# Kernel tuning notes

Measured on AMD Instinct MI355X. Metric: run time of the kernel, lower is better.

The kernel has to match this reference:

```python
import jax, jax.numpy as jnp
import numpy as np

B, N, D, H = 2, 2048, 1024, 16
DK = D // H
SCALE = DK ** -0.5


def setup_inputs() -> dict:
    key = jax.random.key(0)
    ks = jax.random.split(key, 11)
    s = D ** -0.5
    return {
        "q": jax.random.normal(ks[0], (B, N, D), jnp.float32),
        "k": jax.random.normal(ks[1], (B, N, D), jnp.float32),
        "v": jax.random.normal(ks[2], (B, N, D), jnp.float32),
        "Wq": jax.random.normal(ks[3], (D, D), jnp.float32) * s,
        "bq": jnp.zeros((D,), jnp.float32),
        "Wk": jax.random.normal(ks[4], (D, D), jnp.float32) * s,
        "bk": jnp.zeros((D,), jnp.float32),
        "Wv": jax.random.normal(ks[5], (D, D), jnp.float32) * s,
        "bv": jnp.zeros((D,), jnp.float32),
        "Wo": jax.random.normal(ks[6], (D, D), jnp.float32) * s,
        "bo": jnp.zeros((D,), jnp.float32),
    }


def _split_heads(x):
    # [b, n, h*d] -> [b, h, n, d]
    b, n, _ = x.shape
    return x.reshape(b, n, H, DK).transpose(0, 2, 1, 3)


def reference(q, k, v, Wq, bq, Wk, bk, Wv, bv, Wo, bo):
    qh = _split_heads(q @ Wq.T + bq)
    kh = _split_heads(k @ Wk.T + bk)
    vh = _split_heads(v @ Wv.T + bv)
    dots = jnp.einsum('bhid,bhjd->bhij', qh, kh) * SCALE
    attn = jax.nn.softmax(dots, axis=-1)
    out = jnp.einsum('bhij,bhjd->bhid', attn, vh)
    out = out.transpose(0, 2, 1, 3).reshape(q.shape[0], q.shape[1], D)
    return out @ Wo.T + bo
```

## Files before the change

kernel.cpp:

```cpp
#include <hip/hip_runtime.h>
#include <hip/hip_bf16.h>
#include <cstdint>
#include <cstddef>

#define BB 2
#define NN 2048
#define DD 1024
#define HH 16
#define DKK 64
#define SCALE 0.125f
#define LOG2E 1.4426950408889634f

typedef __bf16 bf16;
typedef __bf16 bf16x4 __attribute__((ext_vector_type(4)));
typedef __bf16 bf16x8 __attribute__((ext_vector_type(8)));
typedef float f32x4 __attribute__((ext_vector_type(4)));
typedef short s16x4 __attribute__((ext_vector_type(4)));

#define GLD(gp, lp)                                                            \
  __builtin_amdgcn_global_load_lds(                                            \
      (const __attribute__((address_space(1))) void*)(gp),                     \
      (__attribute__((address_space(3))) void*)(lp), 16, 0, 0)

struct CvtArgs { const float* s[4]; bf16* d[4]; };

__global__ void k_cvtN(CvtArgs a, int n) {
  const float* __restrict__ s = a.s[blockIdx.y];
  bf16* __restrict__ d = a.d[blockIdx.y];
  int i = (blockIdx.x * 256 + threadIdx.x) * 4;
  if (i >= n) return;
  float4 f = *(const float4*)(s + i);
  bf16x4 o;
  o.x = (bf16)f.x; o.y = (bf16)f.y; o.z = (bf16)f.z; o.w = (bf16)f.w;
  *(bf16x4*)(d + i) = o;
}

__device__ __forceinline__ void gemm_body(
    const bf16* __restrict__ A, const bf16* __restrict__ W,
    const float* __restrict__ bias, bf16* __restrict__ outB,
    float* __restrict__ outF, int mode, int m0, int n0) {
  const int K = 1024;
  __shared__ bf16 lA[128 * 32];
  __shared__ bf16 lB[128 * 32];
  const int t = threadIdx.x;
  const int lane = t & 63;
  const int quad = lane >> 4;
  const int l16 = lane & 15;
  const int w = t >> 6;
  const int wm = (w >> 1) * 64;
  const int wn = (w & 1) * 64;

  f32x4 acc[4][4] = {};

  int i0 = t, i1 = t + 256;
  int r0 = i0 >> 2, c0 = (i0 & 3) ^ (r0 & 3);
  int r1 = i1 >> 2, c1 = (i1 & 3) ^ (r1 & 3);
  const bf16* gA0 = A + (size_t)(m0 + r0) * K + c0 * 8;
  const bf16* gA1 = A + (size_t)(m0 + r1) * K + c1 * 8;
  const bf16* gB0 = W + (size_t)(n0 + r0) * K + c0 * 8;
  const bf16* gB1 = W + (size_t)(n0 + r1) * K + c1 * 8;

  const int swzA = (quad ^ (l16 & 3)) * 8;

  for (int kb = 0; kb < K; kb += 32) {
    __syncthreads();
    GLD(gA0 + kb, lA + i0 * 8);
    GLD(gA1 + kb, lA + i1 * 8);
    GLD(gB0 + kb, lB + i0 * 8);
    GLD(gB1 + kb, lB + i1 * 8);
    __syncthreads();

    bf16x8 af[4], bf[4];
#pragma unroll
    for (int i = 0; i < 4; i++) {
      af[i] = *(const bf16x8*)(lA + (wm + i * 16 + l16) * 32 + swzA);
      bf[i] = *(const bf16x8*)(lB + (wn + i * 16 + l16) * 32 + swzA);
    }
#pragma unroll
    for (int mi = 0; mi < 4; mi++)
#pragma unroll
      for (int ni = 0; ni < 4; ni++)
        acc[mi][ni] = __builtin_amdgcn_mfma_f32_16x16x32_bf16(
            af[mi], bf[ni], acc[mi][ni], 0, 0, 0);
  }

#pragma unroll
  for (int mi = 0; mi < 4; mi++) {
#pragma unroll
    for (int ni = 0; ni < 4; ni++) {
#pragma unroll
      for (int r = 0; r < 4; r++) {
        int gm = m0 + wm + mi * 16 + quad * 4 + r;
        int gn = n0 + wn + ni * 16 + l16;
        float v = acc[mi][ni][r] + bias[gn];
        if (mode == 3) {
          outF[(size_t)gm * 1024 + gn] = v;
        } else {
          int b = gm >> 11, row = gm & 2047;
          int h = gn >> 6, dk = gn & 63;
          if (mode == 2)
            outB[((size_t)(b * HH + h) * DKK + dk) * NN + row] = (bf16)v;
          else
            outB[((size_t)(b * HH + h) * NN + row) * DKK + dk] = (bf16)v;
        }
      }
    }
  }
}

__global__ __launch_bounds__(256, 2) void k_gemm(
    const bf16* __restrict__ A, const bf16* __restrict__ W,
    const float* __restrict__ bias, bf16* __restrict__ outB,
    float* __restrict__ outF, int mode) {
  gemm_body(A, W, bias, outB, outF, mode, blockIdx.y * 128, blockIdx.x * 128);
}

struct GemmArgs { const bf16* A[3]; const bf16* W[3]; const float* b[3]; bf16* o[3]; };

__global__ __launch_bounds__(256, 2) void k_gemm3(GemmArgs g) {
  int z = blockIdx.z;
  gemm_body(g.A[z], g.W[z], g.b[z], g.o[z], nullptr, z == 2 ? 2 : 0,
            blockIdx.y * 128, blockIdx.x * 128);
}

__global__ __launch_bounds__(256, 2) void k_attn(
    const bf16* __restrict__ Qp, const bf16* __restrict__ Kp,
    const bf16* __restrict__ Vt, bf16* __restrict__ Ao) {
  __shared__ bf16 lK[128 * 64];
  __shared__ bf16 lV[64 * 128];
  const int t = threadIdx.x;
  const int lane = t & 63;
  const int quad = lane >> 4;
  const int l16 = lane & 15;
  const int w = t >> 6;
  const int bh = blockIdx.y;
  const int qt = blockIdx.x;
  const bf16* Qb = Qp + (size_t)bh * NN * DKK;
  const bf16* Kb = Kp + (size_t)bh * NN * DKK;
  const bf16* Vb = Vt + (size_t)bh * DKK * NN;

  const int qr0 = qt * 128 + w * 32;
  bf16x8 qf[2][2];
#pragma unroll
  for (int j = 0; j < 2; j++)
#pragma unroll
    for (int kq = 0; kq < 2; kq++)
      qf[j][kq] = *(const bf16x8*)(Qb + (size_t)(qr0 + j * 16 + l16) * DKK +
                                   kq * 32 + quad * 8);

  float mj[2] = {-3.0e38f, -3.0e38f}, lj[2] = {0.f, 0.f};
  f32x4 oacc[2][4] = {};
  const float c = SCALE * LOG2E;

  const bf16* gK[4]; const bf16* gV[4];
#pragma unroll
  for (int i4 = 0; i4 < 4; i4++) {
    int i = i4 * 256 + t;
    int rK = i >> 3, cK = (i & 7) ^ (rK & 7);
    gK[i4] = Kb + (size_t)rK * DKK + cK * 8;
    int rV = i >> 4, cV = (i & 15) ^ (rV & 15);
    gV[i4] = Vb + (size_t)rV * NN + cV * 8;
  }
  const int swzK0 = ((quad) ^ (l16 & 7)) * 8;
  const int swzK1 = ((4 + quad) ^ (l16 & 7)) * 8;

  for (int kt = 0; kt < NN; kt += 128) {
    __syncthreads();
#pragma unroll
    for (int i4 = 0; i4 < 4; i4++) {
      GLD(gK[i4] + (size_t)kt * DKK, lK + (i4 * 256 + t) * 8);
      GLD(gV[i4] + kt, lV + (i4 * 256 + t) * 8);
    }
    __syncthreads();

    f32x4 s[2][8];
#pragma unroll
    for (int tt = 0; tt < 8; tt++) {
      const bf16* kbase = lK + (tt * 16 + l16) * 64;
      bf16x8 kf0 = *(const bf16x8*)(kbase + swzK0);
      bf16x8 kf1 = *(const bf16x8*)(kbase + swzK1);
#pragma unroll
      for (int j = 0; j < 2; j++) {
        f32x4 z = {0.f, 0.f, 0.f, 0.f};
        z = __builtin_amdgcn_mfma_f32_16x16x32_bf16(kf0, qf[j][0], z, 0, 0, 0);
        z = __builtin_amdgcn_mfma_f32_16x16x32_bf16(kf1, qf[j][1], z, 0, 0, 0);
        s[j][tt] = z;
      }
    }

    s16x4 pa[2][8];
#pragma unroll
    for (int j = 0; j < 2; j++) {
      float mx = -3.0e38f;
#pragma unroll
      for (int tt = 0; tt < 8; tt++)
#pragma unroll
        for (int r = 0; r < 4; r++) mx = fmaxf(mx, s[j][tt][r]);
      mx = fmaxf(mx, __shfl_xor(mx, 16));
      mx = fmaxf(mx, __shfl_xor(mx, 32));
      float mn = fmaxf(mj[j], mx);
      float al = __builtin_amdgcn_exp2f((mj[j] - mn) * c);
      mj[j] = mn;
      float rs = 0.f;
#pragma unroll
      for (int tt = 0; tt < 8; tt++) {
        bf16x4 pb;
#pragma unroll
        for (int r = 0; r < 4; r++) {
          float p = __builtin_amdgcn_exp2f((s[j][tt][r] - mn) * c);
          rs += p;
          pb[r] = (bf16)p;
        }
        pa[j][tt] = __builtin_bit_cast(s16x4, pb);
      }
      rs += __shfl_xor(rs, 16);
      rs += __shfl_xor(rs, 32);
      lj[j] = lj[j] * al + rs;
      float alr[4];
#pragma unroll
      for (int r = 0; r < 4; r++) alr[r] = __shfl(al, quad * 4 + r);
#pragma unroll
      for (int ni = 0; ni < 4; ni++)
#pragma unroll
        for (int r = 0; r < 4; r++) oacc[j][ni][r] *= alr[r];
    }

#pragma unroll
    for (int tt = 0; tt < 8; tt++) {
#pragma unroll
      for (int ni = 0; ni < 4; ni++) {
        int rv = ni * 16 + l16;
        int cc = 2 * tt + (quad >> 1);
        const bf16* vaddr =
            lV + rv * 128 + ((cc ^ l16) * 8) + (quad & 1) * 4;
        s16x4 vb = __builtin_bit_cast(s16x4, *(const bf16x4*)vaddr);
#pragma unroll
        for (int j = 0; j < 2; j++)
          oacc[j][ni] = __builtin_amdgcn_mfma_f32_16x16x16bf16_1k(
              pa[j][tt], vb, oacc[j][ni], 0, 0, 0);
      }
    }
  }

  const int b = bh >> 4, h = bh & 15;
#pragma unroll
  for (int j = 0; j < 2; j++) {
    float inv[4];
#pragma unroll
    for (int r = 0; r < 4; r++) inv[r] = 1.0f / __shfl(lj[j], quad * 4 + r);
#pragma unroll
    for (int ni = 0; ni < 4; ni++)
#pragma unroll
      for (int r = 0; r < 4; r++) {
        int row = qr0 + j * 16 + quad * 4 + r;
        Ao[(size_t)(b * NN + row) * DD + h * DKK + ni * 16 + l16] =
            (bf16)(oacc[j][ni][r] * inv[r]);
      }
  }
}

extern "C" void kernel_launch(void* const* d_in, const int* in_sizes, int n_in,
                              void* d_out, int out_size, void* d_ws,
                              size_t ws_size, hipStream_t stream) {
  const float* qin = (const float*)d_in[0];
  const float* kin = (const float*)d_in[1];
  const float* vin = (const float*)d_in[2];
  const float* Wq = (const float*)d_in[3];
  const float* bq = (const float*)d_in[4];
  const float* Wk = (const float*)d_in[5];
  const float* bk = (const float*)d_in[6];
  const float* Wv = (const float*)d_in[7];
  const float* bv = (const float*)d_in[8];
  const float* Wo = (const float*)d_in[9];
  const float* bo = (const float*)d_in[10];
  float* out = (float*)d_out;

  const int MN = BB * NN * DD;
  const int WNel = DD * DD;
  bf16* ws = (bf16*)d_ws;

  if (ws_size >= (size_t)(3 * MN + 4 * WNel + 3 * MN) * sizeof(bf16)) {
    bf16* xq = ws;
    bf16* xk = xq + MN;
    bf16* xv = xk + MN;
    bf16* wqb = xv + MN;
    bf16* wkb = wqb + WNel;
    bf16* wvb = wkb + WNel;
    bf16* wob = wvb + WNel;
    bf16* Qp = wob + WNel;
    bf16* Kp = Qp + MN;
    bf16* Vt = Kp + MN;
    bf16* Ao = xq;

    CvtArgs ci{{qin, kin, vin, nullptr}, {xq, xk, xv, nullptr}};
    k_cvtN<<<dim3(MN / 1024, 3), 256, 0, stream>>>(ci, MN);
    CvtArgs cw{{Wq, Wk, Wv, Wo}, {wqb, wkb, wvb, wob}};
    k_cvtN<<<dim3(WNel / 1024, 4), 256, 0, stream>>>(cw, WNel);

    GemmArgs g{{xq, xk, xv}, {wqb, wkb, wvb}, {bq, bk, bv}, {Qp, Kp, Vt}};
    k_gemm3<<<dim3(8, 32, 3), 256, 0, stream>>>(g);

    k_attn<<<dim3(16, 32), 256, 0, stream>>>(Qp, Kp, Vt, Ao);
    k_gemm<<<dim3(8, 32), 256, 0, stream>>>(Ao, wob, bo, nullptr, out, 3);
  } else {
    bf16* xb = ws;
    bf16* wqb = xb + MN;
    bf16* wkb = wqb + WNel;
    bf16* wvb = wkb + WNel;
    bf16* wob = wvb + WNel;
    bf16* Qp = wob + WNel;
    bf16* Kp = Qp + MN;
    bf16* Vt = Kp + MN;

    CvtArgs cw{{Wq, Wk, Wv, Wo}, {wqb, wkb, wvb, wob}};
    k_cvtN<<<dim3(WNel / 1024, 4), 256, 0, stream>>>(cw, WNel);

    CvtArgs c0{{qin, nullptr, nullptr, nullptr}, {xb, nullptr, nullptr, nullptr}};
    k_cvtN<<<dim3(MN / 1024, 1), 256, 0, stream>>>(c0, MN);
    k_gemm<<<dim3(8, 32), 256, 0, stream>>>(xb, wqb, bq, Qp, nullptr, 0);
    CvtArgs c1{{kin, nullptr, nullptr, nullptr}, {xb, nullptr, nullptr, nullptr}};
    k_cvtN<<<dim3(MN / 1024, 1), 256, 0, stream>>>(c1, MN);
    k_gemm<<<dim3(8, 32), 256, 0, stream>>>(xb, wkb, bk, Kp, nullptr, 0);
    CvtArgs c2{{vin, nullptr, nullptr, nullptr}, {xb, nullptr, nullptr, nullptr}};
    k_cvtN<<<dim3(MN / 1024, 1), 256, 0, stream>>>(c2, MN);
    k_gemm<<<dim3(8, 32), 256, 0, stream>>>(xb, wvb, bv, Vt, nullptr, 2);

    k_attn<<<dim3(16, 32), 256, 0, stream>>>(Qp, Kp, Vt, xb);
    k_gemm<<<dim3(8, 32), 256, 0, stream>>>(xb, wob, bo, nullptr, out, 3);
  }
}
```

Measured before the change: 252.9 us.

## Fuse fp32-to-bf16 conversion into GEMMs, double-buffer GEMM and attention

The separate conversion kernels are removed. GEMMs now load fp32 activations and weights, convert them to bf16 in registers and store them into double-buffered LDS with a software prefetch. The softmax scale times log2e is folded into the Q projection output. Attention moves to 512-thread blocks with 16 query rows per wave, double-buffered K/V tiles, a transposed MFMA so each lane writes vectorized output, and a swapped grid order. The output projection uses 128x64 tiles. This removes the conversion passes and exposes more overlap, at the cost of more VGPR and LDS pressure and fp32 weight reads repeated across tiles.

```diff
diff --git a/kernel.cpp b/kernel.cpp
--- a/kernel.cpp
+++ b/kernel.cpp
@@ -22,77 +22,115 @@
       (const __attribute__((address_space(1))) void*)(gp),                     \
       (__attribute__((address_space(3))) void*)(lp), 16, 0, 0)
 
-struct CvtArgs { const float* s[4]; bf16* d[4]; };
-
-__global__ void k_cvtN(CvtArgs a, int n) {
-  const float* __restrict__ s = a.s[blockIdx.y];
-  bf16* __restrict__ d = a.d[blockIdx.y];
-  int i = (blockIdx.x * 256 + threadIdx.x) * 4;
-  if (i >= n) return;
-  float4 f = *(const float4*)(s + i);
-  bf16x4 o;
-  o.x = (bf16)f.x; o.y = (bf16)f.y; o.z = (bf16)f.z; o.w = (bf16)f.w;
-  *(bf16x4*)(d + i) = o;
-}
-
+__device__ __forceinline__ bf16x8 cvt8(float4 a, float4 b) {
+  bf16x8 o;
+  o[0] = (bf16)a.x; o[1] = (bf16)a.y; o[2] = (bf16)a.z; o[3] = (bf16)a.w;
+  o[4] = (bf16)b.x; o[5] = (bf16)b.y; o[6] = (bf16)b.z; o[7] = (bf16)b.w;
+  return o;
+}
+
+template <bool AF32, int BN>
 __device__ __forceinline__ void gemm_body(
-    const bf16* __restrict__ A, const bf16* __restrict__ W,
+    const void* Aptr, const float* __restrict__ Wf,
     const float* __restrict__ bias, bf16* __restrict__ outB,
-    float* __restrict__ outF, int mode, int m0, int n0) {
+    float* __restrict__ outF, int mode, float oscale, int m0, int n0) {
   const int K = 1024;
-  __shared__ bf16 lA[128 * 32];
-  __shared__ bf16 lB[128 * 32];
+  constexpr int NI = BN / 32;
+  __shared__ bf16 lA[2][128 * 32];
+  __shared__ bf16 lB[2][BN * 32];
   const int t = threadIdx.x;
-  const int lane = t & 63;
-  const int quad = lane >> 4;
-  const int l16 = lane & 15;
-  const int w = t >> 6;
-  const int wm = (w >> 1) * 64;
-  const int wn = (w & 1) * 64;
-
-  f32x4 acc[4][4] = {};
-
-  int i0 = t, i1 = t + 256;
-  int r0 = i0 >> 2, c0 = (i0 & 3) ^ (r0 & 3);
-  int r1 = i1 >> 2, c1 = (i1 & 3) ^ (r1 & 3);
-  const bf16* gA0 = A + (size_t)(m0 + r0) * K + c0 * 8;
-  const bf16* gA1 = A + (size_t)(m0 + r1) * K + c1 * 8;
-  const bf16* gB0 = W + (size_t)(n0 + r0) * K + c0 * 8;
-  const bf16* gB1 = W + (size_t)(n0 + r1) * K + c1 * 8;
-
-  const int swzA = (quad ^ (l16 & 3)) * 8;
-
+  const int lane = t & 63, quad = lane >> 4, l16 = lane & 15, w = t >> 6;
+  const int wm = (w >> 1) * 64, wn = (w & 1) * (BN / 2);
+
+  f32x4 acc[4][NI] = {};
+
+  const float* Af = (const float*)Aptr;
+  const bf16* Ab = (const bf16*)Aptr;
+  const int rA = t >> 1, cA = (t & 1) * 16;
+  const int iA0 = t, iA1 = t + 256;
+  const int rG0 = iA0 >> 2, cG0 = (iA0 & 3) ^ (rG0 & 3);
+  const int rG1 = iA1 >> 2, cG1 = (iA1 & 3) ^ (rG1 & 3);
+  const int rW = (BN == 128) ? (t >> 1) : (t >> 2);
+  const int cW = (BN == 128) ? ((t & 1) * 16) : ((t & 3) * 8);
+
+  float4 ar[4];
+  float4 wr[BN == 128 ? 4 : 2];
+
+  auto issueA = [&](int kb, int pp) {
+    if constexpr (AF32) {
+#pragma unroll
+      for (int i = 0; i < 4; i++)
+        ar[i] = *(const float4*)(Af + (size_t)(m0 + rA) * K + kb + cA + i * 4);
+    } else {
+      GLD(Ab + (size_t)(m0 + rG0) * K + kb + cG0 * 8, &lA[pp][iA0 * 8]);
+      GLD(Ab + (size_t)(m0 + rG1) * K + kb + cG1 * 8, &lA[pp][iA1 * 8]);
+    }
+  };
+  auto writeA = [&](int pp) {
+    if constexpr (AF32) {
+      bf16x8 w0 = cvt8(ar[0], ar[1]), w1 = cvt8(ar[2], ar[3]);
+      const int ch0 = cA >> 3;
+      *(bf16x8*)&lA[pp][rA * 32 + ((ch0 ^ (rA & 3)) * 8)] = w0;
+      *(bf16x8*)&lA[pp][rA * 32 + (((ch0 + 1) ^ (rA & 3)) * 8)] = w1;
+    }
+  };
+  auto loadW = [&](int kb) {
+#pragma unroll
+    for (int i = 0; i < (BN == 128 ? 4 : 2); i++)
+      wr[i] = *(const float4*)(Wf + (size_t)(n0 + rW) * K + kb + cW + i * 4);
+  };
+  auto writeW = [&](int pp) {
+    if constexpr (BN == 128) {
+      bf16x8 w0 = cvt8(wr[0], wr[1]), w1 = cvt8(wr[2], wr[3]);
+      const int ch0 = cW >> 3;
+      *(bf16x8*)&lB[pp][rW * 32 + ((ch0 ^ (rW & 3)) * 8)] = w0;
+      *(bf16x8*)&lB[pp][rW * 32 + (((ch0 + 1) ^ (rW & 3)) * 8)] = w1;
+    } else {
+      bf16x8 w0 = cvt8(wr[0], wr[1]);
+      *(bf16x8*)&lB[pp][rW * 32 + ((((cW >> 3)) ^ (rW & 3)) * 8)] = w0;
+    }
+  };
+
+  issueA(0, 0);
+  loadW(0);
+  writeA(0);
+  writeW(0);
+  __syncthreads();
+
+  const int swz = (quad ^ (l16 & 3)) * 8;
+  int p = 0;
   for (int kb = 0; kb < K; kb += 32) {
+    const bool more = kb + 32 < K;
+    if (more) { issueA(kb + 32, p ^ 1); loadW(kb + 32); }
+
+    bf16x8 af[4], bfr[NI];
+#pragma unroll
+    for (int i = 0; i < 4; i++)
+      af[i] = *(const bf16x8*)&lA[p][(wm + i * 16 + l16) * 32 + swz];
+#pragma unroll
+    for (int i = 0; i < NI; i++)
+      bfr[i] = *(const bf16x8*)&lB[p][(wn + i * 16 + l16) * 32 + swz];
+#pragma unroll
+    for (int mi = 0; mi < 4; mi++)
+#pragma unroll
+      for (int ni = 0; ni < NI; ni++)
+        acc[mi][ni] = __builtin_amdgcn_mfma_f32_16x16x32_bf16(
+            af[mi], bfr[ni], acc[mi][ni], 0, 0, 0);
+
+    if (more) { writeA(p ^ 1); writeW(p ^ 1); }
     __syncthreads();
-    GLD(gA0 + kb, lA + i0 * 8);
-    GLD(gA1 + kb, lA + i1 * 8);
-    GLD(gB0 + kb, lB + i0 * 8);
-    GLD(gB1 + kb, lB + i1 * 8);
-    __syncthreads();
-
-    bf16x8 af[4], bf[4];
-#pragma unroll
-    for (int i = 0; i < 4; i++) {
-      af[i] = *(const bf16x8*)(lA + (wm + i * 16 + l16) * 32 + swzA);
-      bf[i] = *(const bf16x8*)(lB + (wn + i * 16 + l16) * 32 + swzA);
-    }
-#pragma unroll
-    for (int mi = 0; mi < 4; mi++)
-#pragma unroll
-      for (int ni = 0; ni < 4; ni++)
-        acc[mi][ni] = __builtin_amdgcn_mfma_f32_16x16x32_bf16(
-            af[mi], bf[ni], acc[mi][ni], 0, 0, 0);
+    p ^= 1;
   }
 
 #pragma unroll
   for (int mi = 0; mi < 4; mi++) {
 #pragma unroll
-    for (int ni = 0; ni < 4; ni++) {
+    for (int ni = 0; ni < NI; ni++) {
 #pragma unroll
       for (int r = 0; r < 4; r++) {
         int gm = m0 + wm + mi * 16 + quad * 4 + r;
         int gn = n0 + wn + ni * 16 + l16;
-        float v = acc[mi][ni][r] + bias[gn];
+        float v = (acc[mi][ni][r] + bias[gn]) * oscale;
         if (mode == 3) {
           outF[(size_t)gm * 1024 + gn] = v;
         } else {
@@ -108,122 +146,120 @@
   }
 }
 
-__global__ __launch_bounds__(256, 2) void k_gemm(
-    const bf16* __restrict__ A, const bf16* __restrict__ W,
-    const float* __restrict__ bias, bf16* __restrict__ outB,
-    float* __restrict__ outF, int mode) {
-  gemm_body(A, W, bias, outB, outF, mode, blockIdx.y * 128, blockIdx.x * 128);
-}
-
-struct GemmArgs { const bf16* A[3]; const bf16* W[3]; const float* b[3]; bf16* o[3]; };
-
-__global__ __launch_bounds__(256, 2) void k_gemm3(GemmArgs g) {
-  int z = blockIdx.z;
-  gemm_body(g.A[z], g.W[z], g.b[z], g.o[z], nullptr, z == 2 ? 2 : 0,
-            blockIdx.y * 128, blockIdx.x * 128);
-}
-
-__global__ __launch_bounds__(256, 2) void k_attn(
+struct QkvArgs {
+  const float* A[3]; const float* W[3]; const float* b[3]; bf16* o[3];
+  float sc[3];
+};
+
+__global__ __launch_bounds__(256, 3) void k_qkv(QkvArgs g) {
+  const int z = blockIdx.z;
+  gemm_body<true, 128>(g.A[z], g.W[z], g.b[z], g.o[z], nullptr,
+                       z == 2 ? 2 : 0, g.sc[z], blockIdx.x * 128,
+                       blockIdx.y * 128);
+}
+
+__global__ __launch_bounds__(256, 3) void k_oproj(
+    const bf16* __restrict__ A, const float* __restrict__ W,
+    const float* __restrict__ bias, float* __restrict__ out) {
+  gemm_body<false, 64>(A, W, bias, nullptr, out, 3, 1.0f, blockIdx.x * 128,
+                       blockIdx.y * 64);
+}
+
+__global__ __launch_bounds__(512, 4) void k_attn(
     const bf16* __restrict__ Qp, const bf16* __restrict__ Kp,
     const bf16* __restrict__ Vt, bf16* __restrict__ Ao) {
-  __shared__ bf16 lK[128 * 64];
-  __shared__ bf16 lV[64 * 128];
+  __shared__ bf16 lK[2][128 * 64];
+  __shared__ bf16 lV[2][64 * 128];
   const int t = threadIdx.x;
-  const int lane = t & 63;
-  const int quad = lane >> 4;
-  const int l16 = lane & 15;
-  const int w = t >> 6;
-  const int bh = blockIdx.y;
-  const int qt = blockIdx.x;
+  const int lane = t & 63, quad = lane >> 4, l16 = lane & 15, w = t >> 6;
+  const int bh = blockIdx.x;
+  const int qt = blockIdx.y;
   const bf16* Qb = Qp + (size_t)bh * NN * DKK;
   const bf16* Kb = Kp + (size_t)bh * NN * DKK;
   const bf16* Vb = Vt + (size_t)bh * DKK * NN;
 
-  const int qr0 = qt * 128 + w * 32;
-  bf16x8 qf[2][2];
-#pragma unroll
-  for (int j = 0; j < 2; j++)
-#pragma unroll
-    for (int kq = 0; kq < 2; kq++)
-      qf[j][kq] = *(const bf16x8*)(Qb + (size_t)(qr0 + j * 16 + l16) * DKK +
-                                   kq * 32 + quad * 8);
-
-  float mj[2] = {-3.0e38f, -3.0e38f}, lj[2] = {0.f, 0.f};
-  f32x4 oacc[2][4] = {};
-  const float c = SCALE * LOG2E;
-
-  const bf16* gK[4]; const bf16* gV[4];
-#pragma unroll
-  for (int i4 = 0; i4 < 4; i4++) {
-    int i = i4 * 256 + t;
+  const int qr0 = qt * 128 + w * 16;
+  bf16x8 qf[2];
+#pragma unroll
+  for (int kq = 0; kq < 2; kq++)
+    qf[kq] = *(const bf16x8*)(Qb + (size_t)(qr0 + l16) * DKK + kq * 32 +
+                              quad * 8);
+
+  float mj = -3.0e38f, lj = 0.f;
+  f32x4 oaccT[4] = {};
+
+  const bf16* gK[2]; const bf16* gV[2];
+#pragma unroll
+  for (int i2 = 0; i2 < 2; i2++) {
+    int i = i2 * 512 + t;
     int rK = i >> 3, cK = (i & 7) ^ (rK & 7);
-    gK[i4] = Kb + (size_t)rK * DKK + cK * 8;
+    gK[i2] = Kb + (size_t)rK * DKK + cK * 8;
     int rV = i >> 4, cV = (i & 15) ^ (rV & 15);
-    gV[i4] = Vb + (size_t)rV * NN + cV * 8;
-  }
-  const int swzK0 = ((quad) ^ (l16 & 7)) * 8;
+    gV[i2] = Vb + (size_t)rV * NN + cV * 8;
+  }
+  const int swzK0 = (quad ^ (l16 & 7)) * 8;
   const int swzK1 = ((4 + quad) ^ (l16 & 7)) * 8;
 
+#pragma unroll
+  for (int i2 = 0; i2 < 2; i2++) {
+    GLD(gK[i2], &lK[0][(i2 * 512 + t) * 8]);
+    GLD(gV[i2], &lV[0][(i2 * 512 + t) * 8]);
+  }
+
+  int p = 0;
   for (int kt = 0; kt < NN; kt += 128) {
     __syncthreads();
-#pragma unroll
-    for (int i4 = 0; i4 < 4; i4++) {
-      GLD(gK[i4] + (size_t)kt * DKK, lK + (i4 * 256 + t) * 8);
-      GLD(gV[i4] + kt, lV + (i4 * 256 + t) * 8);
-    }
-    __syncthreads();
-
-    f32x4 s[2][8];
+    if (kt + 128 < NN) {
+#pragma unroll
+      for (int i2 = 0; i2 < 2; i2++) {
+        GLD(gK[i2] + (size_t)(kt + 128) * DKK, &lK[p ^ 1][(i2 * 512 + t) * 8]);
+        GLD(gV[i2] + (kt + 128), &lV[p ^ 1][(i2 * 512 + t) * 8]);
+      }
+    }
+
+    f32x4 s[8];
 #pragma unroll
     for (int tt = 0; tt < 8; tt++) {
-      const bf16* kbase = lK + (tt * 16 + l16) * 64;
+      const bf16* kbase = &lK[p][(tt * 16 + l16) * 64];
       bf16x8 kf0 = *(const bf16x8*)(kbase + swzK0);
       bf16x8 kf1 = *(const bf16x8*)(kbase + swzK1);
-#pragma unroll
-      for (int j = 0; j < 2; j++) {
-        f32x4 z = {0.f, 0.f, 0.f, 0.f};
-        z = __builtin_amdgcn_mfma_f32_16x16x32_bf16(kf0, qf[j][0], z, 0, 0, 0);
-        z = __builtin_amdgcn_mfma_f32_16x16x32_bf16(kf1, qf[j][1], z, 0, 0, 0);
-        s[j][tt] = z;
+      f32x4 z = {0.f, 0.f, 0.f, 0.f};
+      z = __builtin_amdgcn_mfma_f32_16x16x32_bf16(kf0, qf[0], z, 0, 0, 0);
+      z = __builtin_amdgcn_mfma_f32_16x16x32_bf16(kf1, qf[1], z, 0, 0, 0);
+      s[tt] = z;
+    }
+
+    float mx = -3.0e38f;
+#pragma unroll
+    for (int tt = 0; tt < 8; tt++)
+#pragma unroll
+      for (int r = 0; r < 4; r++) mx = fmaxf(mx, s[tt][r]);
+    mx = fmaxf(mx, __shfl_xor(mx, 16));
+    mx = fmaxf(mx, __shfl_xor(mx, 32));
+    float mn = fmaxf(mj, mx);
+    float al = __builtin_amdgcn_exp2f(mj - mn);
+    mj = mn;
+
+    float rs = 0.f;
+    s16x4 pa[8];
+#pragma unroll
+    for (int tt = 0; tt < 8; tt++) {
+      bf16x4 pb;
+#pragma unroll
+      for (int r = 0; r < 4; r++) {
+        float pe = __builtin_amdgcn_exp2f(s[tt][r] - mn);
+        rs += pe;
+        pb[r] = (bf16)pe;
       }
-    }
-
-    s16x4 pa[2][8];
-#pragma unroll
-    for (int j = 0; j < 2; j++) {
-      float mx = -3.0e38f;
-#pragma unroll
-      for (int tt = 0; tt < 8; tt++)
-#pragma unroll
-        for (int r = 0; r < 4; r++) mx = fmaxf(mx, s[j][tt][r]);
-      mx = fmaxf(mx, __shfl_xor(mx, 16));
-      mx = fmaxf(mx, __shfl_xor(mx, 32));
-      float mn = fmaxf(mj[j], mx);
-      float al = __builtin_amdgcn_exp2f((mj[j] - mn) * c);
-      mj[j] = mn;
-      float rs = 0.f;
-#pragma unroll
-      for (int tt = 0; tt < 8; tt++) {
-        bf16x4 pb;
-#pragma unroll
-        for (int r = 0; r < 4; r++) {
-          float p = __builtin_amdgcn_exp2f((s[j][tt][r] - mn) * c);
-          rs += p;
-          pb[r] = (bf16)p;
-        }
-        pa[j][tt] = __builtin_bit_cast(s16x4, pb);
-      }
-      rs += __shfl_xor(rs, 16);
-      rs += __shfl_xor(rs, 32);
-      lj[j] = lj[j] * al + rs;
-      float alr[4];
-#pragma unroll
-      for (int r = 0; r < 4; r++) alr[r] = __shfl(al, quad * 4 + r);
-#pragma unroll
-      for (int ni = 0; ni < 4; ni++)
-#pragma unroll
-        for (int r = 0; r < 4; r++) oacc[j][ni][r] *= alr[r];
-    }
+      pa[tt] = __builtin_bit_cast(s16x4, pb);
+    }
+    rs += __shfl_xor(rs, 16);
+    rs += __shfl_xor(rs, 32);
+    lj = lj * al + rs;
+#pragma unroll
+    for (int ni = 0; ni < 4; ni++)
+#pragma unroll
+      for (int r = 0; r < 4; r++) oaccT[ni][r] *= al;
 
 #pragma unroll
     for (int tt = 0; tt < 8; tt++) {
@@ -232,30 +268,24 @@
         int rv = ni * 16 + l16;
         int cc = 2 * tt + (quad >> 1);
         const bf16* vaddr =
-            lV + rv * 128 + ((cc ^ l16) * 8) + (quad & 1) * 4;
+            &lV[p][rv * 128 + ((cc ^ l16) * 8) + (quad & 1) * 4];
         s16x4 vb = __builtin_bit_cast(s16x4, *(const bf16x4*)vaddr);
-#pragma unroll
-        for (int j = 0; j < 2; j++)
-          oacc[j][ni] = __builtin_amdgcn_mfma_f32_16x16x16bf16_1k(
-              pa[j][tt], vb, oacc[j][ni], 0, 0, 0);
+        oaccT[ni] = __builtin_amdgcn_mfma_f32_16x16x16bf16_1k(vb, pa[tt],
+                                                              oaccT[ni], 0, 0, 0);
       }
     }
-  }
-
+    p ^= 1;
+  }
+
+  const float inv = 1.0f / lj;
   const int b = bh >> 4, h = bh & 15;
-#pragma unroll
-  for (int j = 0; j < 2; j++) {
-    float inv[4];
-#pragma unroll
-    for (int r = 0; r < 4; r++) inv[r] = 1.0f / __shfl(lj[j], quad * 4 + r);
-#pragma unroll
-    for (int ni = 0; ni < 4; ni++)
-#pragma unroll
-      for (int r = 0; r < 4; r++) {
-        int row = qr0 + j * 16 + quad * 4 + r;
-        Ao[(size_t)(b * NN + row) * DD + h * DKK + ni * 16 + l16] =
-            (bf16)(oacc[j][ni][r] * inv[r]);
-      }
+  bf16* dst = Ao + ((size_t)(b * NN) + qr0 + l16) * DD + h * DKK + quad * 4;
+#pragma unroll
+  for (int ni = 0; ni < 4; ni++) {
+    bf16x4 ov;
+#pragma unroll
+    for (int r = 0; r < 4; r++) ov[r] = (bf16)(oaccT[ni][r] * inv);
+    *(bf16x4*)(dst + ni * 16) = ov;
   }
 }
 
@@ -276,56 +306,16 @@
   float* out = (float*)d_out;
 
   const int MN = BB * NN * DD;
-  const int WNel = DD * DD;
   bf16* ws = (bf16*)d_ws;
-
-  if (ws_size >= (size_t)(3 * MN + 4 * WNel + 3 * MN) * sizeof(bf16)) {
-    bf16* xq = ws;
-    bf16* xk = xq + MN;
-    bf16* xv = xk + MN;
-    bf16* wqb = xv + MN;
-    bf16* wkb = wqb + WNel;
-    bf16* wvb = wkb + WNel;
-    bf16* wob = wvb + WNel;
-    bf16* Qp = wob + WNel;
-    bf16* Kp = Qp + MN;
-    bf16* Vt = Kp + MN;
-    bf16* Ao = xq;
-
-    CvtArgs ci{{qin, kin, vin, nullptr}, {xq, xk, xv, nullptr}};
-    k_cvtN<<<dim3(MN / 1024, 3), 256, 0, stream>>>(ci, MN);
-    CvtArgs cw{{Wq, Wk, Wv, Wo}, {wqb, wkb, wvb, wob}};
-    k_cvtN<<<dim3(WNel / 1024, 4), 256, 0, stream>>>(cw, WNel);
-
-    GemmArgs g{{xq, xk, xv}, {wqb, wkb, wvb}, {bq, bk, bv}, {Qp, Kp, Vt}};
-    k_gemm3<<<dim3(8, 32, 3), 256, 0, stream>>>(g);
-
-    k_attn<<<dim3(16, 32), 256, 0, stream>>>(Qp, Kp, Vt, Ao);
-    k_gemm<<<dim3(8, 32), 256, 0, stream>>>(Ao, wob, bo, nullptr, out, 3);
-  } else {
-    bf16* xb = ws;
-    bf16* wqb = xb + MN;
-    bf16* wkb = wqb + WNel;
-    bf16* wvb = wkb + WNel;
-    bf16* wob = wvb + WNel;
-    bf16* Qp = wob + WNel;
-    bf16* Kp = Qp + MN;
-    bf16* Vt = Kp + MN;
-
-    CvtArgs cw{{Wq, Wk, Wv, Wo}, {wqb, wkb, wvb, wob}};
-    k_cvtN<<<dim3(WNel / 1024, 4), 256, 0, stream>>>(cw, WNel);
-
-    CvtArgs c0{{qin, nullptr, nullptr, nullptr}, {xb, nullptr, nullptr, nullptr}};
-    k_cvtN<<<dim3(MN / 1024, 1), 256, 0, stream>>>(c0, MN);
-    k_gemm<<<dim3(8, 32), 256, 0, stream>>>(xb, wqb, bq, Qp, nullptr, 0);
-    CvtArgs c1{{kin, nullptr, nullptr, nullptr}, {xb, nullptr, nullptr, nullptr}};
-    k_cvtN<<<dim3(MN / 1024, 1), 256, 0, stream>>>(c1, MN);
-    k_gemm<<<dim3(8, 32), 256, 0, stream>>>(xb, wkb, bk, Kp, nullptr, 0);
-    CvtArgs c2{{vin, nullptr, nullptr, nullptr}, {xb, nullptr, nullptr, nullptr}};
-    k_cvtN<<<dim3(MN / 1024, 1), 256, 0, stream>>>(c2, MN);
-    k_gemm<<<dim3(8, 32), 256, 0, stream>>>(xb, wvb, bv, Vt, nullptr, 2);
-
-    k_attn<<<dim3(16, 32), 256, 0, stream>>>(Qp, Kp, Vt, xb);
-    k_gemm<<<dim3(8, 32), 256, 0, stream>>>(xb, wob, bo, nullptr, out, 3);
-  }
-}
+  bf16* Qp = ws;
+  bf16* Kp = Qp + MN;
+  bf16* Vt = Kp + MN;
+  bf16* Ao = Vt + MN;
+
+  const float c = SCALE * LOG2E;
+  QkvArgs g{{qin, kin, vin}, {Wq, Wk, Wv}, {bq, bk, bv}, {Qp, Kp, Vt},
+            {c, 1.0f, 1.0f}};
+  k_qkv<<<dim3(32, 8, 3), 256, 0, stream>>>(g);
+  k_attn<<<dim3(32, 16), 512, 0, stream>>>(Qp, Kp, Vt, Ao);
+  k_oproj<<<dim3(32, 16), 256, 0, stream>>>(Ao, Wo, bo, out);
+}
```

Measured after the change: 267.0 us. +5.6%, slower.
